# Kernel optimization log

Measured on AMD Instinct MI355X. Metric: run time of the kernel, lower is better.

Reference implementation:

```python
import jax, jax.numpy as jnp
import numpy as np

N_NODES = 50000
N_EDGES = 800000
D_NODE = 128
D_EDGE = 64
D_HID = 128  # conv_hiddens[0]


def setup_inputs() -> dict:
    key = jax.random.key(0)
    ks = jax.random.split(key, 12)
    edge_feat = jax.random.normal(ks[0], (N_EDGES, D_EDGE), dtype=jnp.float32)
    node_feat = jax.random.normal(ks[1], (N_NODES, D_NODE), dtype=jnp.float32)
    src = jax.random.randint(ks[2], (N_EDGES,), 0, N_NODES, dtype=jnp.int32)
    dst = jax.random.randint(ks[3], (N_EDGES,), 0, N_NODES, dtype=jnp.int32)
    # attention projections (bias=False), torch Linear stores [out,in]; we use [in,out]
    s_n = 1.0 / np.sqrt(D_NODE)
    Wq = jax.random.normal(ks[4], (D_NODE, D_NODE), dtype=jnp.float32) * s_n
    Wk = jax.random.normal(ks[5], (D_NODE, D_NODE), dtype=jnp.float32) * s_n
    Wv = jax.random.normal(ks[6], (D_NODE, D_NODE), dtype=jnp.float32) * s_n
    # edge MLP: Linear(D_EDGE->D_HID) + act + Linear(D_HID->D_EDGE) + act
    W1 = jax.random.normal(ks[7], (D_EDGE, D_HID), dtype=jnp.float32) * (1.0 / np.sqrt(D_EDGE))
    b1 = jnp.zeros((D_HID,), dtype=jnp.float32)
    W2 = jax.random.normal(ks[8], (D_HID, D_EDGE), dtype=jnp.float32) * (1.0 / np.sqrt(D_HID))
    b2 = jnp.zeros((D_EDGE,), dtype=jnp.float32)
    return {"edge_feat": edge_feat, "node_feat": node_feat, "src": src, "dst": dst,
            "Wq": Wq, "Wk": Wk, "Wv": Wv, "W1": W1, "b1": b1, "W2": W2, "b2": b2}


def reference(edge_feat, node_feat, src, dst, Wq, Wk, Wv, W1, b1, W2, b2):
    act = jax.nn.silu
    n_nodes = node_feat.shape[0]
    d_out = Wq.shape[1]

    # edge MLP (activate_last=True)
    edge_out = act(act(edge_feat @ W1 + b1) @ W2 + b2)

    # single-head node attention
    Q = node_feat @ Wq  # [N, d]
    K = node_feat @ Wk
    V = node_feat @ Wv
    scaling = jnp.sqrt(jnp.asarray(d_out, dtype=node_feat.dtype))
    scores = jnp.sum(Q[dst] * K[src], axis=-1) / scaling  # [E]

    # edge_softmax: softmax over incoming edges of each destination node
    seg_max = jax.ops.segment_max(scores, dst, num_segments=n_nodes)  # [N]
    e = jnp.exp(scores - seg_max[dst])  # [E]
    denom = jax.ops.segment_sum(e, dst, num_segments=n_nodes)  # [N]
    alpha = e / denom[dst]  # [E]

    # weighted scatter-sum of source values to destinations
    node_out = jax.ops.segment_sum(alpha[:, None] * V[src], dst, num_segments=n_nodes)
    return edge_out, node_out
```

## Files before the change

### kernel.cpp

```cpp
#include <hip/hip_runtime.h>
#include <hip/hip_bf16.h>
#include <cstdint>
#include <cstddef>

#define D_NODE 128
#define D_EDGE 64
#define D_HID  128

typedef __attribute__((ext_vector_type(8))) short bf16x8;
typedef __attribute__((ext_vector_type(4))) float f32x4;

__device__ __forceinline__ float silu_f(float x) {
  return x * __builtin_amdgcn_rcpf(1.f + __expf(-x));
}

__device__ __forceinline__ short f2bf(float f) {
  union { float f; uint32_t u; } v; v.f = f;
  uint32_t r = v.u + 0x7fff + ((v.u >> 16) & 1);
  return (short)(r >> 16);
}

__device__ __forceinline__ float bf2f(uint32_t lo16) {
  union { uint32_t u; float f; } v; v.u = lo16 << 16; return v.f;
}

__device__ __forceinline__ uint32_t packkv(float k, float v) {
  return (uint32_t)(uint16_t)f2bf(k) | ((uint32_t)(uint16_t)f2bf(v) << 16);
}

__global__ void prep_weights(const float* __restrict__ W1, const float* __restrict__ W2,
                             short* __restrict__ W1f, short* __restrict__ W2f) {
  const int idx = blockIdx.x * 256 + threadIdx.x;
  if (idx < 1024) {
    const int frag = idx >> 6, lane = idx & 63;
    const int kk = frag >> 3, n = frag & 7;
    const int lg = lane >> 4, lr = lane & 15;
#pragma unroll
    for (int j = 0; j < 8; ++j) {
      const int k = kk * 32 + lg * 8 + j;
      W1f[idx * 8 + j] = f2bf(W1[k * 128 + n * 16 + lr]);
    }
  } else if (idx < 2048) {
    const int t = idx - 1024;
    const int frag = t >> 6, lane = t & 63;
    const int kk = frag >> 2, n = frag & 3;
    const int lg = lane >> 4, lr = lane & 15;
#pragma unroll
    for (int j = 0; j < 8; ++j) {
      const int k = kk * 32 + lg * 8 + j;
      W2f[t * 8 + j] = f2bf(W2[k * 64 + n * 16 + lr]);
    }
  }
}

__global__ __launch_bounds__(256) void edge_mlp_mfma(
    const float* __restrict__ ef, const short* __restrict__ W1f,
    const float* __restrict__ b1, const short* __restrict__ W2f,
    const float* __restrict__ b2, float* __restrict__ out, int E) {
  __shared__ short Hs[128 * 136];

  const int tid = threadIdx.x;
  const int e0 = blockIdx.x * 128;
  const int lane = tid & 63, wave = tid >> 6;
  const int r0 = wave * 32;
  const int lr = lane & 15, lg = lane >> 4;

  float b1v[8], b2v[4];
#pragma unroll
  for (int n = 0; n < 8; ++n) b1v[n] = b1[n * 16 + lr];
#pragma unroll
  for (int n = 0; n < 4; ++n) b2v[n] = b2[n * 16 + lr];

  f32x4 acc1[2][8];
#pragma unroll
  for (int m = 0; m < 2; ++m)
#pragma unroll
    for (int n = 0; n < 8; ++n) acc1[m][n] = (f32x4){0.f, 0.f, 0.f, 0.f};

#pragma unroll
  for (int kk = 0; kk < 2; ++kk) {
    bf16x8 a[2];
#pragma unroll
    for (int m = 0; m < 2; ++m) {
      const int row = e0 + r0 + m * 16 + lr;
      const float* __restrict__ xp = ef + (size_t)row * 64 + kk * 32 + lg * 8;
      float4 f0 = make_float4(0.f, 0.f, 0.f, 0.f), f1 = f0;
      if (row < E) {
        f0 = *reinterpret_cast<const float4*>(xp);
        f1 = *reinterpret_cast<const float4*>(xp + 4);
      }
      a[m][0] = f2bf(f0.x); a[m][1] = f2bf(f0.y); a[m][2] = f2bf(f0.z); a[m][3] = f2bf(f0.w);
      a[m][4] = f2bf(f1.x); a[m][5] = f2bf(f1.y); a[m][6] = f2bf(f1.z); a[m][7] = f2bf(f1.w);
    }
#pragma unroll
    for (int n = 0; n < 8; ++n) {
      const bf16x8 b = *reinterpret_cast<const bf16x8*>(W1f + (((kk << 3) + n) << 9) + (lane << 3));
      acc1[0][n] = __builtin_amdgcn_mfma_f32_16x16x32_bf16(a[0], b, acc1[0][n], 0, 0, 0);
      acc1[1][n] = __builtin_amdgcn_mfma_f32_16x16x32_bf16(a[1], b, acc1[1][n], 0, 0, 0);
    }
  }

#pragma unroll
  for (int m = 0; m < 2; ++m)
#pragma unroll
    for (int n = 0; n < 8; ++n)
#pragma unroll
      for (int r = 0; r < 4; ++r) {
        const float hv = silu_f(acc1[m][n][r] + b1v[n]);
        Hs[(r0 + m * 16 + lg * 4 + r) * 136 + n * 16 + lr] = f2bf(hv);
      }

  f32x4 acc2[2][4];
#pragma unroll
  for (int m = 0; m < 2; ++m)
#pragma unroll
    for (int n = 0; n < 4; ++n) acc2[m][n] = (f32x4){0.f, 0.f, 0.f, 0.f};
#pragma unroll
  for (int kk = 0; kk < 4; ++kk) {
    const bf16x8 a0 = *reinterpret_cast<const bf16x8*>(&Hs[(r0 + lr) * 136 + kk * 32 + lg * 8]);
    const bf16x8 a1 = *reinterpret_cast<const bf16x8*>(&Hs[(r0 + 16 + lr) * 136 + kk * 32 + lg * 8]);
#pragma unroll
    for (int n = 0; n < 4; ++n) {
      const bf16x8 b = *reinterpret_cast<const bf16x8*>(W2f + (((kk << 2) + n) << 9) + (lane << 3));
      acc2[0][n] = __builtin_amdgcn_mfma_f32_16x16x32_bf16(a0, b, acc2[0][n], 0, 0, 0);
      acc2[1][n] = __builtin_amdgcn_mfma_f32_16x16x32_bf16(a1, b, acc2[1][n], 0, 0, 0);
    }
  }
#pragma unroll
  for (int m = 0; m < 2; ++m)
#pragma unroll
    for (int r = 0; r < 4; ++r) {
      const int row = r0 + m * 16 + lg * 4 + r;
      if (e0 + row < E) {
        float* __restrict__ op = out + (size_t)(e0 + row) * 64;
#pragma unroll
        for (int n = 0; n < 4; ++n) op[n * 16 + lr] = silu_f(acc2[m][n][r] + b2v[n]);
      }
    }
}

__global__ __launch_bounds__(256) void qkv_kernel(
    const float* __restrict__ nf, const float* __restrict__ Wq,
    const float* __restrict__ Wk, const float* __restrict__ Wv,
    float* __restrict__ Q, uint32_t* __restrict__ KV, int N) {
  __shared__ float xs[32][D_NODE];
  const int tid = threadIdx.x;
  const int node0 = blockIdx.x * 32;
  const int nrows = min(32, N - node0);
  for (int i = tid; i < nrows * 32; i += 256) {
    const int r = i >> 5, c = (i & 31) * 4;
    float4 v = *reinterpret_cast<const float4*>(nf + (size_t)(node0 + r) * D_NODE + c);
    xs[r][c] = v.x; xs[r][c + 1] = v.y; xs[r][c + 2] = v.z; xs[r][c + 3] = v.w;
  }
  __syncthreads();
  const int wave = tid >> 6, lane = tid & 63;
  const int nn0 = wave * 8;
  float aq[8][2] = {}, ak[8][2] = {}, av[8][2] = {};
  for (int k = 0; k < D_NODE; ++k) {
    const float wq0 = Wq[(k << 7) + lane], wq1 = Wq[(k << 7) + 64 + lane];
    const float wk0 = Wk[(k << 7) + lane], wk1 = Wk[(k << 7) + 64 + lane];
    const float wv0 = Wv[(k << 7) + lane], wv1 = Wv[(k << 7) + 64 + lane];
#pragma unroll
    for (int nn = 0; nn < 8; ++nn) {
      const float x = xs[nn0 + nn][k];
      aq[nn][0] = fmaf(x, wq0, aq[nn][0]); aq[nn][1] = fmaf(x, wq1, aq[nn][1]);
      ak[nn][0] = fmaf(x, wk0, ak[nn][0]); ak[nn][1] = fmaf(x, wk1, ak[nn][1]);
      av[nn][0] = fmaf(x, wv0, av[nn][0]); av[nn][1] = fmaf(x, wv1, av[nn][1]);
    }
  }
#pragma unroll
  for (int nn = 0; nn < 8; ++nn) {
    const int n = node0 + nn0 + nn;
    if (n < N) {
      Q[(size_t)n * 128 + lane] = aq[nn][0]; Q[(size_t)n * 128 + 64 + lane] = aq[nn][1];
      KV[(size_t)n * 128 + lane]      = packkv(ak[nn][0], av[nn][0]);
      KV[(size_t)n * 128 + 64 + lane] = packkv(ak[nn][1], av[nn][1]);
    }
  }
}

__global__ void count_edges(const int* __restrict__ dst, int* __restrict__ counts, int E) {
  const int e = blockIdx.x * blockDim.x + threadIdx.x;
  if (e < E) atomicAdd(&counts[dst[e]], 1);
}

__global__ __launch_bounds__(1024) void scan_pass1(
    const int* __restrict__ counts, int* __restrict__ offsets,
    int* __restrict__ bsums, int n) {
  __shared__ int tmp[1024];
  const int b = blockIdx.x, tid = threadIdx.x;
  const int i = b * 1024 + tid;
  tmp[tid] = (i < n) ? counts[i] : 0;
  __syncthreads();
  for (int off = 1; off < 1024; off <<= 1) {
    const int t = (tid >= off) ? tmp[tid - off] : 0;
    __syncthreads();
    tmp[tid] += t;
    __syncthreads();
  }
  if (i < n) offsets[i + 1] = tmp[tid];
  if (tid == 1023) bsums[b] = tmp[1023];
}

__global__ void scan_pass2(int* __restrict__ bsums, int nb) {
  const int tid = threadIdx.x;
  int v = (tid < nb) ? bsums[tid] : 0;
#pragma unroll
  for (int off = 1; off < 64; off <<= 1) {
    const int t = __shfl_up(v, off);
    if (tid >= off) v += t;
  }
  if (tid < nb) bsums[tid] = v;
}

__global__ __launch_bounds__(1024) void scan_pass3(
    int* __restrict__ offsets, const int* __restrict__ bsums, int n) {
  const int b = blockIdx.x, tid = threadIdx.x;
  const int i = b * 1024 + tid;
  if (b > 0 && i < n) offsets[i + 1] += bsums[b - 1];
  if (b == 0 && tid == 0) offsets[0] = 0;
}

__global__ void scatter_edges(const int* __restrict__ dst, const int* __restrict__ src,
                              const int* __restrict__ offsets,
                              int* __restrict__ cursor, int* __restrict__ esrc, int E) {
  const int e = blockIdx.x * blockDim.x + threadIdx.x;
  if (e >= E) return;
  const int d = dst[e];
  const int pos = atomicAdd(&cursor[d], 1);
  esrc[offsets[d] + pos] = src[e];
}

__global__ __launch_bounds__(256) void node_attn_kernel(
    const float* __restrict__ Q, const uint32_t* __restrict__ KV,
    const int* __restrict__ offsets, const int* __restrict__ esrc,
    float* __restrict__ out, int N) {
  const int lane = threadIdx.x & 63;
  const int n = __builtin_amdgcn_readfirstlane((blockIdx.x * blockDim.x + threadIdx.x) >> 6);
  if (n >= N) return;
  const int beg = offsets[n], end = offsets[n + 1];
  const float scale = 0.088388347648318447f;
  float2 q = *reinterpret_cast<const float2*>(Q + (size_t)n * 128 + lane * 2);
  q.x *= scale; q.y *= scale;
  float m = -3.4e38f, l = 0.f, ax = 0.f, ay = 0.f;

  int p = beg;
  for (; p + 4 <= end; p += 4) {
    const int s0 = esrc[p], s1 = esrc[p + 1], s2 = esrc[p + 2], s3 = esrc[p + 3];
    const uint2 c0 = *reinterpret_cast<const uint2*>(KV + (size_t)s0 * 128 + lane * 2);
    const uint2 c1 = *reinterpret_cast<const uint2*>(KV + (size_t)s1 * 128 + lane * 2);
    const uint2 c2 = *reinterpret_cast<const uint2*>(KV + (size_t)s2 * 128 + lane * 2);
    const uint2 c3 = *reinterpret_cast<const uint2*>(KV + (size_t)s3 * 128 + lane * 2);
    float d0 = q.x * bf2f(c0.x & 0xffff) + q.y * bf2f(c0.y & 0xffff);
    float d1 = q.x * bf2f(c1.x & 0xffff) + q.y * bf2f(c1.y & 0xffff);
    float d2 = q.x * bf2f(c2.x & 0xffff) + q.y * bf2f(c2.y & 0xffff);
    float d3 = q.x * bf2f(c3.x & 0xffff) + q.y * bf2f(c3.y & 0xffff);
#pragma unroll
    for (int off = 32; off > 0; off >>= 1) {
      d0 += __shfl_xor(d0, off);
      d1 += __shfl_xor(d1, off);
      d2 += __shfl_xor(d2, off);
      d3 += __shfl_xor(d3, off);
    }
    const float mx = fmaxf(fmaxf(d0, d1), fmaxf(d2, d3));
    const float mnew = fmaxf(m, mx);
    const float corr = __expf(m - mnew);
    const float p0 = __expf(d0 - mnew), p1 = __expf(d1 - mnew);
    const float p2 = __expf(d2 - mnew), p3 = __expf(d3 - mnew);
    l = l * corr + (p0 + p1 + p2 + p3);
    ax = ax * corr + p0 * bf2f(c0.x >> 16) + p1 * bf2f(c1.x >> 16)
                   + p2 * bf2f(c2.x >> 16) + p3 * bf2f(c3.x >> 16);
    ay = ay * corr + p0 * bf2f(c0.y >> 16) + p1 * bf2f(c1.y >> 16)
                   + p2 * bf2f(c2.y >> 16) + p3 * bf2f(c3.y >> 16);
    m = mnew;
  }
  for (; p < end; ++p) {
    const int s = esrc[p];
    const uint2 c = *reinterpret_cast<const uint2*>(KV + (size_t)s * 128 + lane * 2);
    float part = q.x * bf2f(c.x & 0xffff) + q.y * bf2f(c.y & 0xffff);
#pragma unroll
    for (int off = 32; off > 0; off >>= 1) part += __shfl_xor(part, off);
    const float mnew = fmaxf(m, part);
    const float corr = __expf(m - mnew);
    const float pe = __expf(part - mnew);
    l = l * corr + pe;
    ax = ax * corr + pe * bf2f(c.x >> 16);
    ay = ay * corr + pe * bf2f(c.y >> 16);
    m = mnew;
  }
  const float inv = (end > beg) ? 1.f / l : 0.f;
  float2 o; o.x = ax * inv; o.y = ay * inv;
  *reinterpret_cast<float2*>(out + (size_t)n * 128 + lane * 2) = o;
}

extern "C" void kernel_launch(void* const* d_in, const int* in_sizes, int n_in,
                              void* d_out, int out_size, void* d_ws, size_t ws_size,
                              hipStream_t stream) {
  const float* edge_feat = (const float*)d_in[0];
  const float* node_feat = (const float*)d_in[1];
  const int*   src       = (const int*)d_in[2];
  const int*   dst       = (const int*)d_in[3];
  const float* Wq        = (const float*)d_in[4];
  const float* Wk        = (const float*)d_in[5];
  const float* Wv        = (const float*)d_in[6];
  const float* W1        = (const float*)d_in[7];
  const float* b1        = (const float*)d_in[8];
  const float* W2        = (const float*)d_in[9];
  const float* b2        = (const float*)d_in[10];

  const int E = in_sizes[2];
  const int N = in_sizes[1] / D_NODE;

  float* edge_out = (float*)d_out;
  float* node_out = (float*)d_out + (size_t)E * D_EDGE;

  char* w = (char*)d_ws;
  auto alloc = [&](size_t bytes) {
    char* p = w;
    w += (bytes + 255) & ~(size_t)255;
    return p;
  };
  float*    Q   = (float*)alloc((size_t)N * 128 * sizeof(float));
  uint32_t* KV  = (uint32_t*)alloc((size_t)N * 128 * sizeof(uint32_t));
  int* counts = (int*)alloc((size_t)N * sizeof(int));
  int* cursor = (int*)alloc((size_t)N * sizeof(int));
  int* offs   = (int*)alloc((size_t)(N + 1) * sizeof(int));
  int* esrc   = (int*)alloc((size_t)E * sizeof(int));
  short* W1f  = (short*)alloc(8192 * sizeof(short));
  short* W2f  = (short*)alloc(8192 * sizeof(short));
  int* bsums  = (int*)alloc(64 * sizeof(int));

  hipMemsetAsync(counts, 0, (size_t)((char*)offs - (char*)counts), stream);

  const int nb = (N + 1023) / 1024;
  prep_weights<<<8, 256, 0, stream>>>(W1, W2, W1f, W2f);
  count_edges<<<(E + 255) / 256, 256, 0, stream>>>(dst, counts, E);
  scan_pass1<<<nb, 1024, 0, stream>>>(counts, offs, bsums, N);
  scan_pass2<<<1, 64, 0, stream>>>(bsums, nb);
  scan_pass3<<<nb, 1024, 0, stream>>>(offs, bsums, N);
  scatter_edges<<<(E + 255) / 256, 256, 0, stream>>>(dst, src, offs, cursor, esrc, E);
  qkv_kernel<<<(N + 31) / 32, 256, 0, stream>>>(node_feat, Wq, Wk, Wv, Q, KV, N);
  edge_mlp_mfma<<<(E + 127) / 128, 256, 0, stream>>>(edge_feat, W1f, b1, W2f, b2, edge_out, E);
  node_attn_kernel<<<(N + 3) / 4, 256, 0, stream>>>(Q, KV, offs, esrc, node_out, N);
}
```

Before: 636.4 us.

## Process two nodes per wave in attention and prefill scatter cursors from offsets

The node attention kernel now assigns 32 lanes per node, so each wave handles two nodes. Each lane loads 16-byte KV chunks and the reduction needs one fewer shuffle step, which is meant to halve the per-edge shuffle and latency overhead at low degree (about 16 edges per node). The attention scale moves into the QKV kernel's Q store, and the scatter cursors are seeded by copying the offsets, which removes one dependent offsets load per edge. In exchange there is an extra device copy, and the two half-waves can diverge when their nodes have different degrees.

```diff
diff --git a/kernel.cpp b/kernel.cpp
--- a/kernel.cpp
+++ b/kernel.cpp
@@ -168,11 +168,13 @@
       av[nn][0] = fmaf(x, wv0, av[nn][0]); av[nn][1] = fmaf(x, wv1, av[nn][1]);
     }
   }
+  const float scale = 0.088388347648318447f;
 #pragma unroll
   for (int nn = 0; nn < 8; ++nn) {
     const int n = node0 + nn0 + nn;
     if (n < N) {
-      Q[(size_t)n * 128 + lane] = aq[nn][0]; Q[(size_t)n * 128 + 64 + lane] = aq[nn][1];
+      Q[(size_t)n * 128 + lane]      = aq[nn][0] * scale;
+      Q[(size_t)n * 128 + 64 + lane] = aq[nn][1] * scale;
       KV[(size_t)n * 128 + lane]      = packkv(ak[nn][0], av[nn][0]);
       KV[(size_t)n * 128 + 64 + lane] = packkv(ak[nn][1], av[nn][1]);
     }
@@ -222,41 +224,46 @@
 }
 
 __global__ void scatter_edges(const int* __restrict__ dst, const int* __restrict__ src,
-                              const int* __restrict__ offsets,
                               int* __restrict__ cursor, int* __restrict__ esrc, int E) {
   const int e = blockIdx.x * blockDim.x + threadIdx.x;
   if (e >= E) return;
-  const int d = dst[e];
-  const int pos = atomicAdd(&cursor[d], 1);
-  esrc[offsets[d] + pos] = src[e];
+  const int pos = atomicAdd(&cursor[dst[e]], 1);
+  esrc[pos] = src[e];
 }
 
 __global__ __launch_bounds__(256) void node_attn_kernel(
     const float* __restrict__ Q, const uint32_t* __restrict__ KV,
     const int* __restrict__ offsets, const int* __restrict__ esrc,
     float* __restrict__ out, int N) {
-  const int lane = threadIdx.x & 63;
-  const int n = __builtin_amdgcn_readfirstlane((blockIdx.x * blockDim.x + threadIdx.x) >> 6);
-  if (n >= N) return;
-  const int beg = offsets[n], end = offsets[n + 1];
-  const float scale = 0.088388347648318447f;
-  float2 q = *reinterpret_cast<const float2*>(Q + (size_t)n * 128 + lane * 2);
-  q.x *= scale; q.y *= scale;
-  float m = -3.4e38f, l = 0.f, ax = 0.f, ay = 0.f;
+  const int tid = threadIdx.x;
+  const int lane = tid & 63;
+  const int li = lane & 31;
+  const int n = blockIdx.x * 8 + (tid >> 5);
+  const bool valid = n < N;
+  const int nn = valid ? n : 0;
+  const int beg = offsets[nn];
+  const int end = valid ? offsets[nn + 1] : 0;
+
+  float4 q = *reinterpret_cast<const float4*>(Q + (size_t)nn * 128 + li * 4);
+  float m = -3.4e38f, l = 0.f, a0 = 0.f, a1 = 0.f, a2 = 0.f, a3 = 0.f;
 
   int p = beg;
   for (; p + 4 <= end; p += 4) {
     const int s0 = esrc[p], s1 = esrc[p + 1], s2 = esrc[p + 2], s3 = esrc[p + 3];
-    const uint2 c0 = *reinterpret_cast<const uint2*>(KV + (size_t)s0 * 128 + lane * 2);
-    const uint2 c1 = *reinterpret_cast<const uint2*>(KV + (size_t)s1 * 128 + lane * 2);
-    const uint2 c2 = *reinterpret_cast<const uint2*>(KV + (size_t)s2 * 128 + lane * 2);
-    const uint2 c3 = *reinterpret_cast<const uint2*>(KV + (size_t)s3 * 128 + lane * 2);
-    float d0 = q.x * bf2f(c0.x & 0xffff) + q.y * bf2f(c0.y & 0xffff);
-    float d1 = q.x * bf2f(c1.x & 0xffff) + q.y * bf2f(c1.y & 0xffff);
-    float d2 = q.x * bf2f(c2.x & 0xffff) + q.y * bf2f(c2.y & 0xffff);
-    float d3 = q.x * bf2f(c3.x & 0xffff) + q.y * bf2f(c3.y & 0xffff);
-#pragma unroll
-    for (int off = 32; off > 0; off >>= 1) {
+    const uint4 c0 = *reinterpret_cast<const uint4*>(KV + (size_t)s0 * 128 + li * 4);
+    const uint4 c1 = *reinterpret_cast<const uint4*>(KV + (size_t)s1 * 128 + li * 4);
+    const uint4 c2 = *reinterpret_cast<const uint4*>(KV + (size_t)s2 * 128 + li * 4);
+    const uint4 c3 = *reinterpret_cast<const uint4*>(KV + (size_t)s3 * 128 + li * 4);
+    float d0 = q.x * bf2f(c0.x & 0xffff) + q.y * bf2f(c0.y & 0xffff)
+             + q.z * bf2f(c0.z & 0xffff) + q.w * bf2f(c0.w & 0xffff);
+    float d1 = q.x * bf2f(c1.x & 0xffff) + q.y * bf2f(c1.y & 0xffff)
+             + q.z * bf2f(c1.z & 0xffff) + q.w * bf2f(c1.w & 0xffff);
+    float d2 = q.x * bf2f(c2.x & 0xffff) + q.y * bf2f(c2.y & 0xffff)
+             + q.z * bf2f(c2.z & 0xffff) + q.w * bf2f(c2.w & 0xffff);
+    float d3 = q.x * bf2f(c3.x & 0xffff) + q.y * bf2f(c3.y & 0xffff)
+             + q.z * bf2f(c3.z & 0xffff) + q.w * bf2f(c3.w & 0xffff);
+#pragma unroll
+    for (int off = 16; off > 0; off >>= 1) {
       d0 += __shfl_xor(d0, off);
       d1 += __shfl_xor(d1, off);
       d2 += __shfl_xor(d2, off);
@@ -268,29 +275,38 @@
     const float p0 = __expf(d0 - mnew), p1 = __expf(d1 - mnew);
     const float p2 = __expf(d2 - mnew), p3 = __expf(d3 - mnew);
     l = l * corr + (p0 + p1 + p2 + p3);
-    ax = ax * corr + p0 * bf2f(c0.x >> 16) + p1 * bf2f(c1.x >> 16)
+    a0 = a0 * corr + p0 * bf2f(c0.x >> 16) + p1 * bf2f(c1.x >> 16)
                    + p2 * bf2f(c2.x >> 16) + p3 * bf2f(c3.x >> 16);
-    ay = ay * corr + p0 * bf2f(c0.y >> 16) + p1 * bf2f(c1.y >> 16)
+    a1 = a1 * corr + p0 * bf2f(c0.y >> 16) + p1 * bf2f(c1.y >> 16)
                    + p2 * bf2f(c2.y >> 16) + p3 * bf2f(c3.y >> 16);
+    a2 = a2 * corr + p0 * bf2f(c0.z >> 16) + p1 * bf2f(c1.z >> 16)
+                   + p2 * bf2f(c2.z >> 16) + p3 * bf2f(c3.z >> 16);
+    a3 = a3 * corr + p0 * bf2f(c0.w >> 16) + p1 * bf2f(c1.w >> 16)
+                   + p2 * bf2f(c2.w >> 16) + p3 * bf2f(c3.w >> 16);
     m = mnew;
   }
   for (; p < end; ++p) {
     const int s = esrc[p];
-    const uint2 c = *reinterpret_cast<const uint2*>(KV + (size_t)s * 128 + lane * 2);
-    float part = q.x * bf2f(c.x & 0xffff) + q.y * bf2f(c.y & 0xffff);
-#pragma unroll
-    for (int off = 32; off > 0; off >>= 1) part += __shfl_xor(part, off);
-    const float mnew = fmaxf(m, part);
+    const uint4 c = *reinterpret_cast<const uint4*>(KV + (size_t)s * 128 + li * 4);
+    float d = q.x * bf2f(c.x & 0xffff) + q.y * bf2f(c.y & 0xffff)
+            + q.z * bf2f(c.z & 0xffff) + q.w * bf2f(c.w & 0xffff);
+#pragma unroll
+    for (int off = 16; off > 0; off >>= 1) d += __shfl_xor(d, off);
+    const float mnew = fmaxf(m, d);
     const float corr = __expf(m - mnew);
-    const float pe = __expf(part - mnew);
+    const float pe = __expf(d - mnew);
     l = l * corr + pe;
-    ax = ax * corr + pe * bf2f(c.x >> 16);
-    ay = ay * corr + pe * bf2f(c.y >> 16);
+    a0 = a0 * corr + pe * bf2f(c.x >> 16);
+    a1 = a1 * corr + pe * bf2f(c.y >> 16);
+    a2 = a2 * corr + pe * bf2f(c.z >> 16);
+    a3 = a3 * corr + pe * bf2f(c.w >> 16);
     m = mnew;
   }
-  const float inv = (end > beg) ? 1.f / l : 0.f;
-  float2 o; o.x = ax * inv; o.y = ay * inv;
-  *reinterpret_cast<float2*>(out + (size_t)n * 128 + lane * 2) = o;
+  if (valid) {
+    const float inv = (end > beg) ? 1.f / l : 0.f;
+    float4 o; o.x = a0 * inv; o.y = a1 * inv; o.z = a2 * inv; o.w = a3 * inv;
+    *reinterpret_cast<float4*>(out + (size_t)n * 128 + li * 4) = o;
+  }
 }
 
 extern "C" void kernel_launch(void* const* d_in, const int* in_sizes, int n_in,
@@ -330,7 +346,7 @@
   short* W2f  = (short*)alloc(8192 * sizeof(short));
   int* bsums  = (int*)alloc(64 * sizeof(int));
 
-  hipMemsetAsync(counts, 0, (size_t)((char*)offs - (char*)counts), stream);
+  hipMemsetAsync(counts, 0, (size_t)N * sizeof(int), stream);
 
   const int nb = (N + 1023) / 1024;
   prep_weights<<<8, 256, 0, stream>>>(W1, W2, W1f, W2f);
@@ -338,8 +354,9 @@
   scan_pass1<<<nb, 1024, 0, stream>>>(counts, offs, bsums, N);
   scan_pass2<<<1, 64, 0, stream>>>(bsums, nb);
   scan_pass3<<<nb, 1024, 0, stream>>>(offs, bsums, N);
-  scatter_edges<<<(E + 255) / 256, 256, 0, stream>>>(dst, src, offs, cursor, esrc, E);
+  hipMemcpyAsync(cursor, offs, (size_t)N * sizeof(int), hipMemcpyDeviceToDevice, stream);
+  scatter_edges<<<(E + 255) / 256, 256, 0, stream>>>(dst, src, cursor, esrc, E);
   qkv_kernel<<<(N + 31) / 32, 256, 0, stream>>>(node_feat, Wq, Wk, Wv, Q, KV, N);
   edge_mlp_mfma<<<(E + 127) / 128, 256, 0, stream>>>(edge_feat, W1f, b1, W2f, b2, edge_out, E);
-  node_attn_kernel<<<(N + 3) / 4, 256, 0, stream>>>(Q, KV, offs, esrc, node_out, N);
-}
+  node_attn_kernel<<<(N + 7) / 8, 256, 0, stream>>>(Q, KV, offs, esrc, node_out, N);
+}
```

Result: no change. 646.7 us (+1.6%).
